# Performance work log

Measured on AMD Instinct MI355X. Metric: run time of the kernel, lower is better.

Reference implementation:

```python
import jax, jax.numpy as jnp
import numpy as np

N, D1, D2, B = 8, 2048, 1024, 512
D = D1 * D2
MAXBW = 3
NUM_PART = 5          # num_possible_partitions
TEMP = 0.01           # TEMPERATURE used in df_lt
DENOS = (3.0, 5.0, 17.0)  # 2^2-1, 2^2+1, 2^4+1


def ste_floor(x):
    # straight-through floor: forward floor, backward identity
    return x + jax.lax.stop_gradient(jnp.floor(x) - x)


def segmented_mean(piece, scheme, msp):
    """Replicates the inner python scan over sorted rows.
    piece:  (N, D) sorted residual errors
    scheme: (N-1, D) rounded split decisions (0/1), per column
    msp:    (N-1, D) soft split probabilities (grad factors), per column
    Returns (N, D): each row gets grad_ * (segment mean) of its segment.
    """
    n = piece.shape[0]
    buf = jnp.zeros_like(piece[0])
    cnt = jnp.zeros_like(piece[0])
    g = jnp.ones_like(piece[0])
    reset = jnp.zeros(piece.shape[1], dtype=bool)
    vlist, blist = [], []
    for i in range(n):
        buf = jnp.where(reset, piece[i], buf + piece[i])
        cnt = jnp.where(reset, 1.0, cnt + 1.0)
        g = jnp.where(reset, 1.0, g)
        if i == n - 1:
            vlist.append(g * (buf / cnt))
            blist.append(jnp.ones_like(reset))
        else:
            b = scheme[i] > 0.5
            vlist.append(jnp.where(b, g * msp[i], 0.0) * (buf / cnt))
            blist.append(b)
            g = jnp.where(b, g, g * (1.0 - msp[i]))
            reset = b
    # broadcast each segment-end value back to all rows of its segment
    out = vlist[-1]
    outs = [out]
    for i in range(n - 2, -1, -1):
        out = jnp.where(blist[i], vlist[i], out)
        outs.append(out)
    return jnp.stack(outs[::-1], axis=0)


def residual_quant(U, vsum, s, thr):
    """One residual quantization level (the update_partition=True branch)."""
    res = U - vsum                                   # (N, D)
    idx_maps = jnp.argsort(res, axis=0)              # torch.sort ascending, dim=0
    sorted_err = jnp.take_along_axis(res, idx_maps, axis=0)
    delta = sorted_err[1:] - sorted_err[:-1]         # (N-1, D), >= 0
    delta = delta / jnp.max(delta)
    msp = jax.nn.sigmoid((delta - thr) / TEMP)       # mean_split_point (N-1, D)
    rs = jnp.round(msp)                              # round_split, 0/1

    nm1 = N - 1
    P = 2 ** nm1  # all possible split-column patterns (torch.unique over dim=1)
    weights = (2 ** jnp.arange(nm1 - 1, -1, -1)).astype(jnp.int32)  # row 0 = MSB (lexicographic)
    code = jnp.sum(rs.astype(jnp.int32) * weights[:, None], axis=0)  # (D,)
    counts = jnp.zeros((P,), jnp.int32).at[code].add(1)
    present = counts > 0
    # torch.unique sorts patterns lexicographically -> rank = #present codes below
    rank_of_code = jnp.cumsum(present.astype(jnp.int32)) - present.astype(jnp.int32)
    order = jnp.argsort(-counts)                     # codes by count descending
    top_codes = order[:NUM_PART]
    top_ranks = rank_of_code[top_codes]              # s_indices[:NUM_PART]
    # binary patterns for every possible code
    patterns = ((jnp.arange(P)[:, None] >> jnp.arange(nm1 - 1, -1, -1)[None, :]) & 1).astype(jnp.float32)  # (P, N-1)
    inter = patterns @ patterns[top_codes].T         # (P, NUM_PART)
    sel = jnp.argmax(inter, axis=1)
    reassigned = top_ranks[sel]                      # (P,)
    is_top = jnp.any(rank_of_code[:, None] == top_ranks[None, :], axis=1)
    final_rank = jnp.where(is_top, rank_of_code, reassigned)  # (P,)
    c_rank = final_rank[code]                        # clustered_indices, (D,)

    # NOTE: original indexes round_split / mean_split_point columns BY the
    # unique-cluster index value s_idx (a quirk of the source); replicate it.
    scheme_used = rs[:, c_rank]                      # (N-1, D)
    msp_used = msp[:, c_rank]                        # (N-1, D)

    inner = segmented_mean(sorted_err, scheme_used, msp_used)  # (N, D)
    # einsum('cb,cba->ab', inner, one_hot(idx_maps)) == unsort along dim 0
    inv = jnp.argsort(idx_maps, axis=0)
    grouped = jnp.take_along_axis(inner, inv, axis=0)
    return s * ste_floor(grouped / s)


def setup_inputs():
    key = jax.random.key(0)
    k1, k2 = jax.random.split(key)
    x = jax.random.normal(k1, (B, N, D1), dtype=jnp.float32)
    # kaiming_normal_ on (N, D): std = sqrt(2 / fan_in), fan_in = D
    U = jax.random.normal(k2, (N, D), dtype=jnp.float32) * np.float32(np.sqrt(2.0 / D))
    thres_mean = jnp.full((D2,), -1.3, dtype=jnp.float32)
    return {"x": x, "U": U, "thres_mean": thres_mean}


def reference(x, U, thres_mean):
    beta = jnp.max(U)
    alpha = jnp.min(U)
    s = (beta - alpha) / DENOS[0]
    vsum = s * ste_floor(U / s)                      # base quantization level
    thr = jax.nn.sigmoid(jnp.repeat(thres_mean, D1))  # thres_mean.repeat_interleave(D1)
    for deno in DENOS[1:MAXBW]:
        s = s / deno
        vsum = vsum + residual_quant(U, vsum, s, thr)
    w = vsum.reshape(N, D1, D2)
    return jnp.einsum('bnd,ndl->bnl', x, w)
```

## Files before the change

kernel.cpp:

```cpp
#include <hip/hip_runtime.h>
#include <hip/hip_bf16.h>
#include <math.h>

#define NROW 8
#define DT   2097152
#define DD1  2048
#define DD2  1024
#define BATCH 512
#define NBLK 2048


#define SL_SMAX 0
#define SL_SMIN 2048
#define SL_G2   4096
#define SL_G3   6144

typedef __attribute__((ext_vector_type(8))) short short8;
typedef __attribute__((ext_vector_type(4))) float f32x4;

__device__ __forceinline__ unsigned fenc(float f){
  unsigned u = __float_as_uint(f);
  return (u & 0x80000000u) ? ~u : (u | 0x80000000u);
}
__device__ __forceinline__ float fdec(unsigned k){
  return (k & 0x80000000u) ? __uint_as_float(k ^ 0x80000000u) : __uint_as_float(~k);
}
__device__ __forceinline__ float sigmoid_ref(float z){
  #pragma clang fp contract(off)
  return 1.0f / (1.0f + expf(-z));
}
__device__ __forceinline__ unsigned short f2bf(float f){
  __hip_bfloat16 h = __float2bfloat16(f);
  return *reinterpret_cast<unsigned short*>(&h);
}
__device__ __forceinline__ float base1(float u, float s1, float inv_s1){
  #pragma clang fp contract(off)
  return s1 * floorf(u * inv_s1);
}
__device__ __forceinline__ float vn2_of(float u, unsigned char mb, float s1, float inv_s1, float s2){
  #pragma clang fp contract(off)
  return base1(u, s1, inv_s1) + s2 * (float)((int)mb - 8);
}
__device__ __forceinline__ void async16(const unsigned short* g, unsigned short* l){
  __builtin_amdgcn_global_load_lds((const __attribute__((address_space(1))) unsigned int*)g,
                                   (__attribute__((address_space(3))) unsigned int*)l, 16, 0, 0);
}

#define CSWAPV(a,b) { float _lo=fminf(a,b), _hi=fmaxf(a,b); a=_lo; b=_hi; }
__device__ __forceinline__ void sort8v(float v[8]){
  CSWAPV(v[0],v[1]) CSWAPV(v[2],v[3]) CSWAPV(v[4],v[5]) CSWAPV(v[6],v[7])
  CSWAPV(v[0],v[2]) CSWAPV(v[1],v[3]) CSWAPV(v[4],v[6]) CSWAPV(v[5],v[7])
  CSWAPV(v[1],v[2]) CSWAPV(v[5],v[6])
  CSWAPV(v[0],v[4]) CSWAPV(v[1],v[5]) CSWAPV(v[2],v[6]) CSWAPV(v[3],v[7])
  CSWAPV(v[2],v[4]) CSWAPV(v[3],v[5])
  CSWAPV(v[1],v[2]) CSWAPV(v[3],v[4]) CSWAPV(v[5],v[6])
}
__device__ __forceinline__ void cswapkv(float&av,int&ai,float&bv,int&bi){
  bool sw = (av > bv) || ((av == bv) && (ai > bi));
  float nav = sw ? bv : av; float nbv = sw ? av : bv;
  int   nai = sw ? bi : ai; int   nbi = sw ? ai : bi;
  av = nav; bv = nbv; ai = nai; bi = nbi;
}
#define CSWAPK(i,j) cswapkv(v[i],ix[i],v[j],ix[j]);
__device__ __forceinline__ void sort8kv(float v[8], int ix[8]){
  CSWAPK(0,1) CSWAPK(2,3) CSWAPK(4,5) CSWAPK(6,7)
  CSWAPK(0,2) CSWAPK(1,3) CSWAPK(4,6) CSWAPK(5,7)
  CSWAPK(1,2) CSWAPK(5,6)
  CSWAPK(0,4) CSWAPK(1,5) CSWAPK(2,6) CSWAPK(3,7)
  CSWAPK(2,4) CSWAPK(3,5)
  CSWAPK(1,2) CSWAPK(3,4) CSWAPK(5,6)
}

__global__ __launch_bounds__(256) void k_mmxb(const float* __restrict__ U, const float* __restrict__ x,
                                              unsigned short* __restrict__ xb,
                                              unsigned* __restrict__ meta, unsigned* __restrict__ slots){
  __shared__ unsigned redA[256], redB[256];
  int t = threadIdx.x, b = blockIdx.x;
  int gid = b*256 + t;
  if (b == 0 && t < 128){ meta[4+t] = 0u; meta[132+t] = 0u; }
  const float4* x4 = (const float4*)x;
  #pragma unroll
  for (int i = 0; i < 4; ++i){
    int idx = gid + i*524288;
    float4 v = x4[idx];
    ushort4 o;
    o.x = f2bf(v.x); o.y = f2bf(v.y); o.z = f2bf(v.z); o.w = f2bf(v.w);
    *(ushort4*)(xb + (size_t)idx*4) = o;
  }
  const float4* U4 = (const float4*)U;
  float mx = -INFINITY, mn = INFINITY;
  #pragma unroll
  for (int i = 0; i < 8; ++i){
    float4 v = U4[gid + i*524288];
    mx = fmaxf(mx, fmaxf(fmaxf(v.x,v.y), fmaxf(v.z,v.w)));
    mn = fminf(mn, fminf(fminf(v.x,v.y), fminf(v.z,v.w)));
  }
  redA[t] = fenc(mx); redB[t] = fenc(mn);
  __syncthreads();
  for (int o = 128; o > 0; o >>= 1){
    if (t < o){ redA[t] = max(redA[t], redA[t+o]); redB[t] = min(redB[t], redB[t+o]); }
    __syncthreads();
  }
  if (t == 0){ slots[SL_SMAX + b] = redA[0]; slots[SL_SMIN + b] = redB[0]; }
}

template<int MODE>
__global__ void k_fin(const unsigned* __restrict__ slots, unsigned* __restrict__ fin){
  __shared__ unsigned redA[256], redB[256];
  int t = threadIdx.x;
  if (MODE == 0){
    unsigned vx = 0u, vn = 0xFFFFFFFFu;
    for (int i = t; i < NBLK; i += 256){ vx = max(vx, slots[SL_SMAX+i]); vn = min(vn, slots[SL_SMIN+i]); }
    redA[t] = vx; redB[t] = vn;
    __syncthreads();
    for (int o = 128; o > 0; o >>= 1){
      if (t < o){ redA[t] = max(redA[t], redA[t+o]); redB[t] = min(redB[t], redB[t+o]); }
      __syncthreads();
    }
    if (t == 0){
      float s1 = (fdec(redA[0]) - fdec(redB[0])) / 3.0f;
      fin[0] = __float_as_uint(s1);
    }
  } else {
    const unsigned* s = slots + ((MODE==1) ? SL_G2 : SL_G3);
    unsigned vx = 0u;
    for (int i = t; i < NBLK; i += 256) vx = max(vx, s[i]);
    redA[t] = vx;
    __syncthreads();
    for (int o = 128; o > 0; o >>= 1){
      if (t < o) redA[t] = max(redA[t], redA[t+o]);
      __syncthreads();
    }
    if (t == 0) fin[MODE] = redA[0];
  }
}

__global__ __launch_bounds__(256) void k_passA2(const float* __restrict__ U,
                                                const unsigned* __restrict__ fin,
                                                unsigned* __restrict__ slots){
  #pragma clang fp contract(off)
  __shared__ unsigned red[256];
  int t = threadIdx.x, b = blockIdx.x;
  float s1 = __uint_as_float(fin[0]);
  float inv_s1 = 1.0f / s1;
  int d0 = (b*256 + t)*4;
  float4 u[8];
  #pragma unroll
  for (int i = 0; i < 8; ++i) u[i] = *(const float4*)(U + (size_t)i*DT + d0);
  unsigned dmax = 0u;
  #pragma unroll
  for (int c = 0; c < 4; ++c){
    float res[8];
    #pragma unroll
    for (int i = 0; i < 8; ++i){
      float uv = ((const float*)&u[i])[c];
      res[i] = uv - base1(uv, s1, inv_s1);
    }
    sort8v(res);
    float m = 0.0f;
    #pragma unroll
    for (int i = 0; i < 7; ++i) m = fmaxf(m, res[i+1] - res[i]);
    dmax = max(dmax, __float_as_uint(m));
  }
  red[t] = dmax;
  __syncthreads();
  for (int o = 128; o > 0; o >>= 1){
    if (t < o) red[t] = max(red[t], red[t+o]);
    __syncthreads();
  }
  if (t == 0) slots[SL_G2 + b] = red[0];
}

template<int LEVEL>
__global__ __launch_bounds__(256) void k_passB(const float* __restrict__ U,
                                               const unsigned char* __restrict__ mcode,
                                               const float* __restrict__ tm,
                                               unsigned char* __restrict__ code,
                                               unsigned* __restrict__ meta,
                                               const unsigned* __restrict__ fin){
  #pragma clang fp contract(off)
  __shared__ int hist[128];
  int t = threadIdx.x, b = blockIdx.x;
  int lane = t & 63;
  if (t < 128) hist[t] = 0;
  float s1 = __uint_as_float(fin[0]);
  float inv_s1 = 1.0f / s1;
  float s2 = s1 / 5.0f;
  float gmax = __uint_as_float(fin[(LEVEL==2)?1:2]);
  float inv_gmax = 1.0f / gmax;
  int d0 = (b*256 + t)*4;
  float4 u[8], bb[8];
  #pragma unroll
  for (int i = 0; i < 8; ++i){
    u[i] = *(const float4*)(U + (size_t)i*DT + d0);
    if (LEVEL == 2){
      bb[i].x = base1(u[i].x, s1, inv_s1); bb[i].y = base1(u[i].y, s1, inv_s1);
      bb[i].z = base1(u[i].z, s1, inv_s1); bb[i].w = base1(u[i].w, s1, inv_s1);
    } else {
      uchar4 m4 = *(const uchar4*)(mcode + (size_t)i*DT + d0);
      bb[i].x = vn2_of(u[i].x, m4.x, s1, inv_s1, s2);
      bb[i].y = vn2_of(u[i].y, m4.y, s1, inv_s1, s2);
      bb[i].z = vn2_of(u[i].z, m4.z, s1, inv_s1, s2);
      bb[i].w = vn2_of(u[i].w, m4.w, s1, inv_s1, s2);
    }
  }
  __syncthreads();
  float thr = sigmoid_ref(tm[d0 >> 11]);
  uchar4 cods;
  unsigned char* cp = (unsigned char*)&cods;
  #pragma unroll
  for (int c = 0; c < 4; ++c){
    float res[8];
    #pragma unroll
    for (int i = 0; i < 8; ++i) res[i] = ((const float*)&u[i])[c] - ((const float*)&bb[i])[c];
    sort8v(res);
    int cd = 0;
    #pragma unroll
    for (int i = 0; i < 7; ++i){
      float dn = (res[i+1] - res[i]) * inv_gmax;
      cd = (cd << 1) | ((dn > thr) ? 1 : 0);
    }
    cp[c] = (unsigned char)cd;
    bool pending = true;
    while (true){
      unsigned long long nd = __ballot(pending);
      if (nd == 0ull) break;
      int leader = (int)__ffsll((unsigned long long)nd) - 1;
      int lc = __shfl(cd, leader);
      bool mine = pending && (cd == lc);
      unsigned long long mm = __ballot(mine);
      if (lane == leader) atomicAdd(&hist[lc], (int)__popcll(mm));
      if (mine) pending = false;
    }
  }
  *(uchar4*)(code + d0) = cods;
  __syncthreads();
  if (t < 128){ int h = hist[t]; if (h) atomicAdd((int*)&meta[((LEVEL==2)?4:132) + t], h); }
}

template<int LEVEL>
__global__ void k_small(const float* __restrict__ U, const unsigned char* __restrict__ mcode,
                        const float* __restrict__ tm, unsigned* __restrict__ meta,
                        const unsigned* __restrict__ fin){
  #pragma clang fp contract(off)
  __shared__ int cs[128], rk[128], redk[128];
  __shared__ int top_code[5], top_rank[5];
  __shared__ int w0cnt;
  int c = threadIdx.x;
  float s1 = __uint_as_float(fin[0]);
  float inv_s1 = 1.0f / s1;
  float s2 = s1 / 5.0f;
  float gmax = __uint_as_float(fin[(LEVEL==2)?1:2]);
  cs[c] = (int)meta[((LEVEL==2)?4:132) + c];
  bool present = cs[c] > 0;
  unsigned long long bm = __ballot(present);
  int lane = c & 63;
  int r = (int)__popcll(bm & ((1ull << lane) - 1ull));
  if (c == 63) w0cnt = (int)__popcll(bm);
  __syncthreads();
  if (c >= 64) r += w0cnt;
  rk[c] = r;
  __syncthreads();
  for (int k = 0; k < 5; ++k){
    redk[c] = (cs[c] << 7) | (127 - c);
    __syncthreads();
    for (int o = 64; o > 0; o >>= 1){
      if (c < o) redk[c] = max(redk[c], redk[c+o]);
      __syncthreads();
    }
    if (c == 0){
      int best = 127 - (redk[0] & 127);
      top_code[k] = best; top_rank[k] = rk[best];
      cs[best] = -1;
    }
    __syncthreads();
  }
  int besti = -1, sel = 0;
  #pragma unroll
  for (int j = 0; j < 5; ++j){
    int inter = __popc(c & top_code[j]);
    if (inter > besti){ besti = inter; sel = j; }
  }
  bool is_top = false;
  #pragma unroll
  for (int j = 0; j < 5; ++j) is_top = is_top || (rk[c] == top_rank[j]);
  ((int*)meta)[260 + c] = is_top ? rk[c] : top_rank[sel];
  float res[8];
  #pragma unroll
  for (int i = 0; i < 8; ++i){
    size_t off = (size_t)i*DT + c;
    float u = U[off];
    float bval = (LEVEL==2) ? base1(u, s1, inv_s1) : vn2_of(u, mcode[off], s1, inv_s1, s2);
    res[i] = u - bval;
  }
  sort8v(res);
  float thr = sigmoid_ref(tm[c >> 11]);
  unsigned bits = 0;
  float* msp_tab = (float*)(meta + 388);
  #pragma unroll
  for (int i = 0; i < 7; ++i){
    float dn  = (res[i+1] - res[i]) / gmax;
    float z   = (dn - thr) / 0.01f;
    float msp = sigmoid_ref(z);
    msp_tab[c*7 + i] = msp;
    bits |= ((unsigned)(int)rintf(msp)) << i;
  }
  meta[1284 + c] = bits;
}

template<int LEVEL>
__global__ __launch_bounds__(256) void k_passD(const float* __restrict__ U,
                                               unsigned char* __restrict__ mcode,
                                               unsigned short* __restrict__ vsumb,
                                               const unsigned char* __restrict__ code,
                                               unsigned* __restrict__ meta,
                                               const unsigned* __restrict__ fin,
                                               unsigned* __restrict__ slots){
  #pragma clang fp contract(off)
  __shared__ float q_lds[32*256];
  __shared__ unsigned red[256];
  __shared__ int fr_s[128];
  __shared__ unsigned bits_s[128];
  __shared__ float msp_s[896];
  int t = threadIdx.x, b = blockIdx.x;
  float s1 = __uint_as_float(fin[0]);
  float inv_s1 = 1.0f / s1;
  float s2 = s1 / 5.0f;
  float s  = (LEVEL == 2) ? s2 : (s2 / 17.0f);
  float inv_s = 1.0f / s;
  if (t < 128){ fr_s[t] = ((const int*)meta)[260+t]; bits_s[t] = meta[1284+t]; }
  for (int i = t; i < 896; i += 256) msp_s[i] = ((const float*)(meta+388))[i];
  __syncthreads();
  int d0 = (b*256 + t)*4;
  float4 u4[8], b4[8];
  #pragma unroll
  for (int i = 0; i < 8; ++i){
    u4[i] = *(const float4*)(U + (size_t)i*DT + d0);
    if (LEVEL == 2){
      b4[i].x = base1(u4[i].x, s1, inv_s1); b4[i].y = base1(u4[i].y, s1, inv_s1);
      b4[i].z = base1(u4[i].z, s1, inv_s1); b4[i].w = base1(u4[i].w, s1, inv_s1);
    } else {
      uchar4 m4 = *(const uchar4*)(mcode + (size_t)i*DT + d0);
      b4[i].x = vn2_of(u4[i].x, m4.x, s1, inv_s1, s2);
      b4[i].y = vn2_of(u4[i].y, m4.y, s1, inv_s1, s2);
      b4[i].z = vn2_of(u4[i].z, m4.z, s1, inv_s1, s2);
      b4[i].w = vn2_of(u4[i].w, m4.w, s1, inv_s1, s2);
    }
  }
  uchar4 cods = *(const uchar4*)(code + d0);
  const unsigned char* cp = (const unsigned char*)&cods;
  #pragma unroll
  for (int c = 0; c < 4; ++c){
    float v[8]; int ix[8];
    #pragma unroll
    for (int i = 0; i < 8; ++i){
      v[i] = ((const float*)&u4[i])[c] - ((const float*)&b4[i])[c];
      ix[i] = i;
    }
    sort8kv(v, ix);
    int cr = fr_s[cp[c]];
    unsigned sb = bits_s[cr];
    float vv[8]; bool bl[8];
    float buf = 0.0f, cnt = 0.0f, g = 1.0f; bool reset = false;
    #pragma unroll
    for (int i = 0; i < 8; ++i){
      buf = reset ? v[i] : (buf + v[i]);
      cnt = reset ? 1.0f : (cnt + 1.0f);
      g   = reset ? 1.0f : g;
      float m = buf * __builtin_amdgcn_rcpf(cnt);
      if (i == 7){ vv[7] = g * m; bl[7] = true; }
      else {
        float msp = msp_s[cr*7 + i];
        bool bv = ((sb >> i) & 1u) != 0u;
        vv[i] = bv ? ((g * msp) * m) : 0.0f;
        bl[i] = bv;
        g = bv ? g : (g * (1.0f - msp));
        reset = bv;
      }
    }
    float out = vv[7];
    float inner[8];
    inner[7] = out;
    for (int i = 6; i >= 0; --i){ if (bl[i]) out = vv[i]; inner[i] = out; }
    #pragma unroll
    for (int i = 0; i < 8; ++i){
      float mf = floorf(inner[i] * inv_s);
      q_lds[(ix[i]*4 + c)*256 + t] = mf;
    }
  }
  unsigned dmax = 0u;
  if (LEVEL == 2){
    uchar4 mout[8];
    #pragma unroll
    for (int c = 0; c < 4; ++c){
      float res3[8];
      #pragma unroll
      for (int rr = 0; rr < 8; ++rr){
        int mi = (int)q_lds[(rr*4 + c)*256 + t];
        mi = max(-8, min(7, mi));
        float q = s * (float)mi;
        float vn = ((const float*)&b4[rr])[c] + q;
        ((unsigned char*)&mout[rr])[c] = (unsigned char)(mi + 8);
        res3[rr] = ((const float*)&u4[rr])[c] - vn;
      }
      sort8v(res3);
      float m = 0.0f;
      #pragma unroll
      for (int i = 0; i < 7; ++i) m = fmaxf(m, res3[i+1] - res3[i]);
      dmax = max(dmax, __float_as_uint(m));
    }
    #pragma unroll
    for (int rr = 0; rr < 8; ++rr)
      *(uchar4*)(mcode + (size_t)rr*DT + d0) = mout[rr];
    __syncthreads();
    red[t] = dmax;
    __syncthreads();
    for (int o = 128; o > 0; o >>= 1){
      if (t < o) red[t] = max(red[t], red[t+o]);
      __syncthreads();
    }
    if (t == 0) slots[SL_G3 + b] = red[0];
  } else {
    #pragma unroll
    for (int rr = 0; rr < 8; ++rr){
      ushort4 o;
      #pragma unroll
      for (int c = 0; c < 4; ++c){
        float q = s * q_lds[(rr*4 + c)*256 + t];
        float vn = ((const float*)&b4[rr])[c] + q;
        ((unsigned short*)&o)[c] = f2bf(vn);
      }
      *(ushort4*)(vsumb + (size_t)rr*DT + d0) = o;
    }
  }
}

__global__ __launch_bounds__(256) void k_wt(const unsigned short* __restrict__ vsumb,
                                            unsigned short* __restrict__ wt){
  __shared__ unsigned short tile[64][68];
  int t = threadIdx.x;
  int c4 = t & 15, r0 = t >> 4;
  int n = blockIdx.z, k0 = blockIdx.y*64, l0 = blockIdx.x*64;
  const unsigned short* src = vsumb + (size_t)n*DT;
  #pragma unroll
  for (int i = 0; i < 4; ++i){
    int r = r0 + i*16;
    ushort4 v = *(const ushort4*)(src + (size_t)(k0+r)*DD2 + l0 + c4*4);
    *(ushort4*)&tile[r][c4*4] = v;
  }
  __syncthreads();
  unsigned short* dst = wt + (size_t)n*DT;
  #pragma unroll
  for (int i = 0; i < 4; ++i){
    int rl = r0 + i*16;
    ushort4 o;
    o.x = tile[c4*4+0][rl]; o.y = tile[c4*4+1][rl];
    o.z = tile[c4*4+2][rl]; o.w = tile[c4*4+3][rl];
    *(ushort4*)(dst + (size_t)(l0+rl)*DD1 + k0 + c4*4) = o;
  }
}

__global__ __launch_bounds__(256) void k_gemm(const unsigned short* __restrict__ xb,
                                              const unsigned short* __restrict__ wt,
                                              float* __restrict__ out){
  __shared__ __align__(16) unsigned short As[64*64];
  __shared__ __align__(16) unsigned short Bs[128*64];
  int t = threadIdx.x;
  int lane = t & 63, wv = t >> 6;
  int n  = blockIdx.z;
  int b0 = blockIdx.y * 64;
  int l0 = blockIdx.x * 128;
  int wm = (wv >> 1) * 32, wn = (wv & 1) * 64;
  int col = lane & 15, quad = lane >> 4;
  int arow = lane >> 3, aseg = lane & 7;
  const unsigned short* wtn = wt + (size_t)n*DT;
  f32x4 acc[2][4] = {};
  for (int k0 = 0; k0 < DD1; k0 += 64){
    #pragma unroll
    for (int i = 0; i < 2; ++i){
      int row = wv*16 + i*8 + arow;
      const unsigned short* g = xb + (((size_t)(b0+row)*NROW + n)*DD1 + k0 + aseg*8);
      async16(g, &As[(wv*16 + i*8)*64]);
    }
    #pragma unroll
    for (int i = 0; i < 4; ++i){
      int row = wv*32 + i*8 + arow;
      const unsigned short* g = wtn + ((size_t)(l0+row)*DD1 + k0 + aseg*8);
      async16(g, &Bs[(wv*32 + i*8)*64]);
    }
    __syncthreads();
    #pragma unroll
    for (int ks = 0; ks < 2; ++ks){
      int kq = ks*32 + quad*8;
      short8 af[2], bfr[4];
      #pragma unroll
      for (int mi = 0; mi < 2; ++mi) af[mi]  = *(const short8*)&As[(wm + mi*16 + col)*64 + kq];
      #pragma unroll
      for (int ni = 0; ni < 4; ++ni) bfr[ni] = *(const short8*)&Bs[(wn + ni*16 + col)*64 + kq];
      #pragma unroll
      for (int mi = 0; mi < 2; ++mi)
        #pragma unroll
        for (int ni = 0; ni < 4; ++ni)
          acc[mi][ni] = __builtin_amdgcn_mfma_f32_16x16x32_bf16(af[mi], bfr[ni], acc[mi][ni], 0, 0, 0);
    }
    __syncthreads();
  }
  #pragma unroll
  for (int mi = 0; mi < 2; ++mi)
    #pragma unroll
    for (int ni = 0; ni < 4; ++ni)
      #pragma unroll
      for (int r = 0; r < 4; ++r){
        int bb = b0 + wm + mi*16 + quad*4 + r;
        int l = l0 + wn + ni*16 + col;
        out[((size_t)bb*NROW + n)*DD2 + l] = acc[mi][ni][r];
      }
}

extern "C" void kernel_launch(void* const* d_in, const int* in_sizes, int n_in,
                              void* d_out, int out_size, void* d_ws, size_t ws_size,
                              hipStream_t stream){
  const float* x  = (const float*)d_in[0];
  const float* U  = (const float*)d_in[1];
  const float* tm = (const float*)d_in[2];
  float* out = (float*)d_out;
  unsigned char*  mcode = (unsigned char*)d_ws;
  unsigned short* vsumb = (unsigned short*)((unsigned char*)d_ws + 16777216);
  unsigned short* xb    = (unsigned short*)((unsigned char*)d_ws + 50331648);
  unsigned char*  code  = (unsigned char*)d_ws + 67108864;
  unsigned short* wt    = (unsigned short*)((unsigned char*)d_ws + 69206016);
  unsigned* meta  = (unsigned*)((unsigned char*)d_ws + 102760448);
  unsigned* slots = (unsigned*)((unsigned char*)d_ws + 102768640);
  unsigned* fin   = (unsigned*)((unsigned char*)d_ws + 102801408);
  (void)in_sizes; (void)n_in; (void)out_size; (void)ws_size;

  k_mmxb    <<<NBLK, 256, 0, stream>>>(U, x, xb, meta, slots);
  k_fin<0>  <<<1,    256, 0, stream>>>(slots, fin);
  k_passA2  <<<NBLK, 256, 0, stream>>>(U, fin, slots);
  k_fin<1>  <<<1,    256, 0, stream>>>(slots, fin);
  k_passB<2><<<NBLK, 256, 0, stream>>>(U, mcode, tm, code, meta, fin);
  k_small<2><<<1,   128, 0, stream>>>(U, mcode, tm, meta, fin);
  k_passD<2><<<NBLK, 256, 0, stream>>>(U, mcode, vsumb, code, meta, fin, slots);
  k_fin<2>  <<<1,    256, 0, stream>>>(slots, fin);
  k_passB<3><<<NBLK, 256, 0, stream>>>(U, mcode, tm, code, meta, fin);
  k_small<3><<<1,   128, 0, stream>>>(U, mcode, tm, meta, fin);
  k_passD<3><<<NBLK, 256, 0, stream>>>(U, mcode, vsumb, code, meta, fin, slots);
  k_wt  <<<dim3(DD2/64, DD1/64, NROW), 256, 0, stream>>>(vsumb, wt);
  k_gemm<<<dim3(DD2/128, BATCH/64, NROW), 256, 0, stream>>>(xb, wt, out);
}
```

Before: 384.2 us.

## Replace per-block slot reductions with global atomics and shrink passD LDS usage

Block-level partial max/min values are now merged directly into the fin array with atomicMax/atomicMin, which removes the three single-block k_fin kernels and their launches. The fin array is reset with two memsets instead. The passB histogram uses a 7-ballot match mask instead of a leader loop, and passD recomputes base values per column with a much smaller LDS buffer, which should help occupancy. The cost is global atomic contention (2048 per pass), extra memset launches, and repeated base1 computation.

```diff
diff --git a/kernel.cpp b/kernel.cpp
--- a/kernel.cpp
+++ b/kernel.cpp
@@ -9,11 +9,6 @@
 #define BATCH 512
 #define NBLK 2048
 
-
-#define SL_SMAX 0
-#define SL_SMIN 2048
-#define SL_G2   4096
-#define SL_G3   6144
 
 typedef __attribute__((ext_vector_type(8))) short short8;
 typedef __attribute__((ext_vector_type(4))) float f32x4;
@@ -73,7 +68,7 @@
 
 __global__ __launch_bounds__(256) void k_mmxb(const float* __restrict__ U, const float* __restrict__ x,
                                               unsigned short* __restrict__ xb,
-                                              unsigned* __restrict__ meta, unsigned* __restrict__ slots){
+                                              unsigned* __restrict__ meta, unsigned* __restrict__ fin){
   __shared__ unsigned redA[256], redB[256];
   int t = threadIdx.x, b = blockIdx.x;
   int gid = b*256 + t;
@@ -101,47 +96,15 @@
     if (t < o){ redA[t] = max(redA[t], redA[t+o]); redB[t] = min(redB[t], redB[t+o]); }
     __syncthreads();
   }
-  if (t == 0){ slots[SL_SMAX + b] = redA[0]; slots[SL_SMIN + b] = redB[0]; }
-}
-
-template<int MODE>
-__global__ void k_fin(const unsigned* __restrict__ slots, unsigned* __restrict__ fin){
-  __shared__ unsigned redA[256], redB[256];
-  int t = threadIdx.x;
-  if (MODE == 0){
-    unsigned vx = 0u, vn = 0xFFFFFFFFu;
-    for (int i = t; i < NBLK; i += 256){ vx = max(vx, slots[SL_SMAX+i]); vn = min(vn, slots[SL_SMIN+i]); }
-    redA[t] = vx; redB[t] = vn;
-    __syncthreads();
-    for (int o = 128; o > 0; o >>= 1){
-      if (t < o){ redA[t] = max(redA[t], redA[t+o]); redB[t] = min(redB[t], redB[t+o]); }
-      __syncthreads();
-    }
-    if (t == 0){
-      float s1 = (fdec(redA[0]) - fdec(redB[0])) / 3.0f;
-      fin[0] = __float_as_uint(s1);
-    }
-  } else {
-    const unsigned* s = slots + ((MODE==1) ? SL_G2 : SL_G3);
-    unsigned vx = 0u;
-    for (int i = t; i < NBLK; i += 256) vx = max(vx, s[i]);
-    redA[t] = vx;
-    __syncthreads();
-    for (int o = 128; o > 0; o >>= 1){
-      if (t < o) redA[t] = max(redA[t], redA[t+o]);
-      __syncthreads();
-    }
-    if (t == 0) fin[MODE] = redA[0];
-  }
+  if (t == 0){ atomicMax(&fin[0], redA[0]); atomicMin(&fin[3], redB[0]); }
 }
 
 __global__ __launch_bounds__(256) void k_passA2(const float* __restrict__ U,
-                                                const unsigned* __restrict__ fin,
-                                                unsigned* __restrict__ slots){
+                                                unsigned* __restrict__ fin){
   #pragma clang fp contract(off)
   __shared__ unsigned red[256];
   int t = threadIdx.x, b = blockIdx.x;
-  float s1 = __uint_as_float(fin[0]);
+  float s1 = (fdec(fin[0]) - fdec(fin[3])) / 3.0f;
   float inv_s1 = 1.0f / s1;
   int d0 = (b*256 + t)*4;
   float4 u[8];
@@ -168,7 +131,7 @@
     if (t < o) red[t] = max(red[t], red[t+o]);
     __syncthreads();
   }
-  if (t == 0) slots[SL_G2 + b] = red[0];
+  if (t == 0) atomicMax(&fin[1], red[0]);
 }
 
 template<int LEVEL>
@@ -183,7 +146,7 @@
   int t = threadIdx.x, b = blockIdx.x;
   int lane = t & 63;
   if (t < 128) hist[t] = 0;
-  float s1 = __uint_as_float(fin[0]);
+  float s1 = (fdec(fin[0]) - fdec(fin[3])) / 3.0f;
   float inv_s1 = 1.0f / s1;
   float s2 = s1 / 5.0f;
   float gmax = __uint_as_float(fin[(LEVEL==2)?1:2]);
@@ -221,17 +184,15 @@
       cd = (cd << 1) | ((dn > thr) ? 1 : 0);
     }
     cp[c] = (unsigned char)cd;
-    bool pending = true;
-    while (true){
-      unsigned long long nd = __ballot(pending);
-      if (nd == 0ull) break;
-      int leader = (int)__ffsll((unsigned long long)nd) - 1;
-      int lc = __shfl(cd, leader);
-      bool mine = pending && (cd == lc);
-      unsigned long long mm = __ballot(mine);
-      if (lane == leader) atomicAdd(&hist[lc], (int)__popcll(mm));
-      if (mine) pending = false;
-    }
+    unsigned long long mset = ~0ull;
+    #pragma unroll
+    for (int bi = 0; bi < 7; ++bi){
+      bool bit = ((cd >> bi) & 1) != 0;
+      unsigned long long bbm = __ballot(bit);
+      mset &= bit ? bbm : ~bbm;
+    }
+    int leader = (int)__ffsll(mset) - 1;
+    if (lane == leader) atomicAdd(&hist[cd], (int)__popcll(mset));
   }
   *(uchar4*)(code + d0) = cods;
   __syncthreads();
@@ -247,7 +208,7 @@
   __shared__ int top_code[5], top_rank[5];
   __shared__ int w0cnt;
   int c = threadIdx.x;
-  float s1 = __uint_as_float(fin[0]);
+  float s1 = (fdec(fin[0]) - fdec(fin[3])) / 3.0f;
   float inv_s1 = 1.0f / s1;
   float s2 = s1 / 5.0f;
   float gmax = __uint_as_float(fin[(LEVEL==2)?1:2]);
@@ -314,16 +275,15 @@
                                                unsigned short* __restrict__ vsumb,
                                                const unsigned char* __restrict__ code,
                                                unsigned* __restrict__ meta,
-                                               const unsigned* __restrict__ fin,
-                                               unsigned* __restrict__ slots){
-  #pragma clang fp contract(off)
-  __shared__ float q_lds[32*256];
+                                               unsigned* __restrict__ fin){
+  #pragma clang fp contract(off)
+  __shared__ float qcol[8*256];
   __shared__ unsigned red[256];
   __shared__ int fr_s[128];
   __shared__ unsigned bits_s[128];
   __shared__ float msp_s[896];
   int t = threadIdx.x, b = blockIdx.x;
-  float s1 = __uint_as_float(fin[0]);
+  float s1 = (fdec(fin[0]) - fdec(fin[3])) / 3.0f;
   float inv_s1 = 1.0f / s1;
   float s2 = s1 / 5.0f;
   float s  = (LEVEL == 2) ? s2 : (s2 / 17.0f);
@@ -332,29 +292,31 @@
   for (int i = t; i < 896; i += 256) msp_s[i] = ((const float*)(meta+388))[i];
   __syncthreads();
   int d0 = (b*256 + t)*4;
-  float4 u4[8], b4[8];
+  float4 u4[8];
+  uchar4 m4[8];
   #pragma unroll
   for (int i = 0; i < 8; ++i){
     u4[i] = *(const float4*)(U + (size_t)i*DT + d0);
-    if (LEVEL == 2){
-      b4[i].x = base1(u4[i].x, s1, inv_s1); b4[i].y = base1(u4[i].y, s1, inv_s1);
-      b4[i].z = base1(u4[i].z, s1, inv_s1); b4[i].w = base1(u4[i].w, s1, inv_s1);
-    } else {
-      uchar4 m4 = *(const uchar4*)(mcode + (size_t)i*DT + d0);
-      b4[i].x = vn2_of(u4[i].x, m4.x, s1, inv_s1, s2);
-      b4[i].y = vn2_of(u4[i].y, m4.y, s1, inv_s1, s2);
-      b4[i].z = vn2_of(u4[i].z, m4.z, s1, inv_s1, s2);
-      b4[i].w = vn2_of(u4[i].w, m4.w, s1, inv_s1, s2);
-    }
+    if (LEVEL == 3) m4[i] = *(const uchar4*)(mcode + (size_t)i*DT + d0);
   }
   uchar4 cods = *(const uchar4*)(code + d0);
   const unsigned char* cp = (const unsigned char*)&cods;
+  uchar4 mout[8];
+  ushort4 ov[8];
+  unsigned dmax = 0u;
   #pragma unroll
   for (int c = 0; c < 4; ++c){
     float v[8]; int ix[8];
     #pragma unroll
     for (int i = 0; i < 8; ++i){
-      v[i] = ((const float*)&u4[i])[c] - ((const float*)&b4[i])[c];
+      float uv = ((const float*)&u4[i])[c];
+      float bval;
+      if (LEVEL == 2) bval = base1(uv, s1, inv_s1);
+      else {
+        int mi = (int)((const unsigned char*)&m4[i])[c] - 8;
+        bval = base1(uv, s1, inv_s1) + s2 * (float)mi;
+      }
+      v[i] = uv - bval;
       ix[i] = i;
     }
     sort8kv(v, ix);
@@ -382,56 +344,58 @@
     float inner[8];
     inner[7] = out;
     for (int i = 6; i >= 0; --i){ if (bl[i]) out = vv[i]; inner[i] = out; }
-    #pragma unroll
-    for (int i = 0; i < 8; ++i){
-      float mf = floorf(inner[i] * inv_s);
-      q_lds[(ix[i]*4 + c)*256 + t] = mf;
-    }
-  }
-  unsigned dmax = 0u;
-  if (LEVEL == 2){
-    uchar4 mout[8];
-    #pragma unroll
-    for (int c = 0; c < 4; ++c){
+    if (LEVEL == 2){
+      unsigned mp = 0u;
+      #pragma unroll
+      for (int i = 0; i < 8; ++i){
+        float mf = floorf(inner[i] * inv_s);
+        int mi = (int)mf;
+        mi = max(-8, min(7, mi));
+        mp |= (unsigned)(mi + 8) << (4*ix[i]);
+      }
       float res3[8];
       #pragma unroll
-      for (int rr = 0; rr < 8; ++rr){
-        int mi = (int)q_lds[(rr*4 + c)*256 + t];
-        mi = max(-8, min(7, mi));
-        float q = s * (float)mi;
-        float vn = ((const float*)&b4[rr])[c] + q;
-        ((unsigned char*)&mout[rr])[c] = (unsigned char)(mi + 8);
-        res3[rr] = ((const float*)&u4[rr])[c] - vn;
+      for (int r = 0; r < 8; ++r){
+        int mi = (int)((mp >> (4*r)) & 15u) - 8;
+        ((unsigned char*)&mout[r])[c] = (unsigned char)(mi + 8);
+        float uv = ((const float*)&u4[r])[c];
+        float qv = s * (float)mi;
+        float vn = base1(uv, s1, inv_s1) + qv;
+        res3[r] = uv - vn;
       }
       sort8v(res3);
       float m = 0.0f;
       #pragma unroll
       for (int i = 0; i < 7; ++i) m = fmaxf(m, res3[i+1] - res3[i]);
       dmax = max(dmax, __float_as_uint(m));
-    }
-    #pragma unroll
-    for (int rr = 0; rr < 8; ++rr)
-      *(uchar4*)(mcode + (size_t)rr*DT + d0) = mout[rr];
-    __syncthreads();
+    } else {
+      #pragma unroll
+      for (int i = 0; i < 8; ++i) qcol[ix[i]*256 + t] = floorf(inner[i] * inv_s);
+      #pragma unroll
+      for (int r = 0; r < 8; ++r){
+        int mi = (int)((const unsigned char*)&m4[r])[c] - 8;
+        float uv = ((const float*)&u4[r])[c];
+        float bv = base1(uv, s1, inv_s1) + s2 * (float)mi;
+        float qv = s * qcol[r*256 + t];
+        ((unsigned short*)&ov[r])[c] = f2bf(bv + qv);
+      }
+    }
+  }
+  if (LEVEL == 2){
+    #pragma unroll
+    for (int r = 0; r < 8; ++r)
+      *(uchar4*)(mcode + (size_t)r*DT + d0) = mout[r];
     red[t] = dmax;
     __syncthreads();
     for (int o = 128; o > 0; o >>= 1){
       if (t < o) red[t] = max(red[t], red[t+o]);
       __syncthreads();
     }
-    if (t == 0) slots[SL_G3 + b] = red[0];
+    if (t == 0) atomicMax(&fin[2], red[0]);
   } else {
     #pragma unroll
-    for (int rr = 0; rr < 8; ++rr){
-      ushort4 o;
-      #pragma unroll
-      for (int c = 0; c < 4; ++c){
-        float q = s * q_lds[(rr*4 + c)*256 + t];
-        float vn = ((const float*)&b4[rr])[c] + q;
-        ((unsigned short*)&o)[c] = f2bf(vn);
-      }
-      *(ushort4*)(vsumb + (size_t)rr*DT + d0) = o;
-    }
+    for (int r = 0; r < 8; ++r)
+      *(ushort4*)(vsumb + (size_t)r*DT + d0) = ov[r];
   }
 }
 
@@ -530,21 +494,19 @@
   unsigned char*  code  = (unsigned char*)d_ws + 67108864;
   unsigned short* wt    = (unsigned short*)((unsigned char*)d_ws + 69206016);
   unsigned* meta  = (unsigned*)((unsigned char*)d_ws + 102760448);
-  unsigned* slots = (unsigned*)((unsigned char*)d_ws + 102768640);
   unsigned* fin   = (unsigned*)((unsigned char*)d_ws + 102801408);
   (void)in_sizes; (void)n_in; (void)out_size; (void)ws_size;
 
-  k_mmxb    <<<NBLK, 256, 0, stream>>>(U, x, xb, meta, slots);
-  k_fin<0>  <<<1,    256, 0, stream>>>(slots, fin);
-  k_passA2  <<<NBLK, 256, 0, stream>>>(U, fin, slots);
-  k_fin<1>  <<<1,    256, 0, stream>>>(slots, fin);
+  hipMemsetAsync(fin, 0, 12, stream);
+  hipMemsetAsync(fin + 3, 0xFF, 4, stream);
+  k_mmxb    <<<NBLK, 256, 0, stream>>>(U, x, xb, meta, fin);
+  k_passA2  <<<NBLK, 256, 0, stream>>>(U, fin);
   k_passB<2><<<NBLK, 256, 0, stream>>>(U, mcode, tm, code, meta, fin);
   k_small<2><<<1,   128, 0, stream>>>(U, mcode, tm, meta, fin);
-  k_passD<2><<<NBLK, 256, 0, stream>>>(U, mcode, vsumb, code, meta, fin, slots);
-  k_fin<2>  <<<1,    256, 0, stream>>>(slots, fin);
+  k_passD<2><<<NBLK, 256, 0, stream>>>(U, mcode, vsumb, code, meta, fin);
   k_passB<3><<<NBLK, 256, 0, stream>>>(U, mcode, tm, code, meta, fin);
   k_small<3><<<1,   128, 0, stream>>>(U, mcode, tm, meta, fin);
-  k_passD<3><<<NBLK, 256, 0, stream>>>(U, mcode, vsumb, code, meta, fin, slots);
+  k_passD<3><<<NBLK, 256, 0, stream>>>(U, mcode, vsumb, code, meta, fin);
   k_wt  <<<dim3(DD2/64, DD1/64, NROW), 256, 0, stream>>>(vsumb, wt);
   k_gemm<<<dim3(DD2/128, BATCH/64, NROW), 256, 0, stream>>>(xb, wt, out);
 }
```

New measurement: 401.3 us. +4.5%, slower.
